# Performance work log

Hardware: AMD Instinct MI355X
Metric: run time of the kernel (lower is better)

## Reference

```python
import jax, jax.numpy as jnp
import numpy as np

N = 50000
E_RAND = 800000
F_IN = 512
HID = 64
HEADS = 4
C = 40
NEG_SLOPE = 0.2  # PyG GATConv default leaky_relu slope


def setup_inputs() -> dict:
    key = jax.random.key(0)
    ks = jax.random.split(key, 12)
    x = jax.random.normal(ks[0], (N, F_IN), dtype=jnp.float32)
    # random edges + self loops (PyG GATConv add_self_loops=True)
    ei_rand = jax.random.randint(ks[1], (2, E_RAND), 0, N, dtype=jnp.int64)
    loops = jnp.broadcast_to(jnp.arange(N, dtype=jnp.int64), (2, N))
    edge_index = jnp.concatenate([ei_rand, loops], axis=1)  # [2, 850000]
    # layer 1: F_IN -> HEADS*HID, concat
    s1 = 1.0 / np.sqrt(F_IN)
    W1 = jax.random.normal(ks[2], (F_IN, HEADS * HID), dtype=jnp.float32) * s1
    a_src1 = jax.random.normal(ks[3], (HEADS, HID), dtype=jnp.float32) * (1.0 / np.sqrt(HID))
    a_dst1 = jax.random.normal(ks[4], (HEADS, HID), dtype=jnp.float32) * (1.0 / np.sqrt(HID))
    b1 = jnp.zeros((HEADS * HID,), dtype=jnp.float32)
    # layer 2: HEADS*HID -> C, 1 head, concat=False
    s2 = 1.0 / np.sqrt(HEADS * HID)
    W2 = jax.random.normal(ks[5], (HEADS * HID, C), dtype=jnp.float32) * s2
    a_src2 = jax.random.normal(ks[6], (1, C), dtype=jnp.float32) * (1.0 / np.sqrt(C))
    a_dst2 = jax.random.normal(ks[7], (1, C), dtype=jnp.float32) * (1.0 / np.sqrt(C))
    b2 = jnp.zeros((C,), dtype=jnp.float32)
    return {"x": x, "edge_index": edge_index, "W1": W1, "a_src1": a_src1,
            "a_dst1": a_dst1, "b1": b1, "W2": W2, "a_src2": a_src2,
            "a_dst2": a_dst2, "b2": b2}


def gat_conv(x, src, dst, W, a_s, a_d, b, concat):
    n = x.shape[0]
    H, D = a_s.shape
    h = (x @ W).reshape(n, H, D)                    # [N,H,D]
    al_s = jnp.einsum('nhd,hd->nh', h, a_s)          # per-node src score
    al_d = jnp.einsum('nhd,hd->nh', h, a_d)          # per-node dst score
    e = jax.nn.leaky_relu(al_s[src] + al_d[dst], NEG_SLOPE)  # [E,H]
    # segment softmax over edges grouped by destination node
    m = jax.ops.segment_max(e, dst, num_segments=n)  # [N,H]
    e = jnp.exp(e - m[dst])
    denom = jax.ops.segment_sum(e, dst, num_segments=n)
    alpha = e / (denom[dst] + 1e-16)                 # [E,H]
    msg = h[src] * alpha[:, :, None]                 # [E,H,D]
    out = jax.ops.segment_sum(msg, dst, num_segments=n)  # [N,H,D]
    out = out.reshape(n, H * D) if concat else out.mean(axis=1)
    return out + b


def reference(x, edge_index, W1, a_src1, a_dst1, b1, W2, a_src2, a_dst2, b2):
    src, dst = edge_index[0], edge_index[1]
    # dropout p=0.6 is identity in eval mode
    h = jax.nn.elu(gat_conv(x, src, dst, W1, a_src1, a_dst1, b1, concat=True))
    out = gat_conv(h, src, dst, W2, a_src2, a_dst2, b2, concat=False)
    return jax.nn.log_softmax(out, axis=1)
```

## Files before the change

kernel.cpp:

```cpp
#include <hip/hip_runtime.h>
#include <math.h>

#define NNODES 50000
#define NPAD 50176
#define FIN 512
#define HID 64
#define HEADS 4
#define HD (HEADS * HID)
#define NCLS 40
#define NCLSP 64
#define NEG_SLOPE 0.2f
#define SBLK 256
#define NSCAN ((NNODES + SBLK - 1) / SBLK)

typedef __attribute__((ext_vector_type(8))) short short8;
typedef __attribute__((ext_vector_type(4))) float f32x4;

static __device__ inline unsigned short f2bf(float f) {
    unsigned int u = __builtin_bit_cast(unsigned int, f);
    unsigned int r = (u + 0x7FFFu + ((u >> 16) & 1u)) >> 16;
    return (unsigned short)r;
}
static __device__ inline float bf2f(unsigned short b) {
    return __builtin_bit_cast(float, (unsigned int)b << 16);
}
static __device__ inline void gload_lds16(const unsigned short* g, unsigned short* l) {
    __builtin_amdgcn_global_load_lds(
        (const __attribute__((address_space(1))) unsigned int*)g,
        (__attribute__((address_space(3))) unsigned int*)l, 16, 0, 0);
}

__global__ __launch_bounds__(256) void xcast_kernel(const float* __restrict__ x,
                                                    unsigned short* __restrict__ xb) {
    const size_t idx = ((size_t)blockIdx.x * 256 + threadIdx.x) * 8;
    if (idx < (size_t)NNODES * FIN) {
        const float4 v0 = *(const float4*)&x[idx];
        const float4 v1 = *(const float4*)&x[idx + 4];
        ushort4 p0, p1;
        p0.x = f2bf(v0.x); p0.y = f2bf(v0.y); p0.z = f2bf(v0.z); p0.w = f2bf(v0.w);
        p1.x = f2bf(v1.x); p1.y = f2bf(v1.y); p1.z = f2bf(v1.z); p1.w = f2bf(v1.w);
        *(ushort4*)&xb[idx] = p0;
        *(ushort4*)&xb[idx + 4] = p1;
    } else {
        const ushort4 z = {0, 0, 0, 0};
        *(ushort4*)&xb[idx] = z;
        *(ushort4*)&xb[idx + 4] = z;
    }
}

__global__ __launch_bounds__(256) void w1t_kernel(const float* __restrict__ W1,
                                                  unsigned short* __restrict__ W1t) {
    const int idx = blockIdx.x * 256 + threadIdx.x;
    const int k = idx >> 8;
    const int n = idx & 255;
    W1t[n * FIN + k] = f2bf(W1[idx]);
}

__global__ __launch_bounds__(256) void w2t_kernel(const float* __restrict__ W2,
                                                  unsigned short* __restrict__ W2t) {
    const int idx = blockIdx.x * 256 + threadIdx.x;
    const int n = idx >> 8;
    const int k = idx & 255;
    W2t[n * HD + k] = (n < NCLS) ? f2bf(W2[k * NCLS + n]) : (unsigned short)0;
}

#define BM 64
#define BN 256
#define BK 32

__global__ __launch_bounds__(256) void gemm1_kernel(const unsigned short* __restrict__ xb,
                                                    const unsigned short* __restrict__ W1t,
                                                    const float* __restrict__ a_src,
                                                    const float* __restrict__ a_dst,
                                                    unsigned short* __restrict__ h1,
                                                    float* __restrict__ al_s,
                                                    float* __restrict__ al_d) {
    __shared__ unsigned short As[BM * BK];
    __shared__ unsigned short Bs[BN * BK];
    const int tid = threadIdx.x;
    const int wave = tid >> 6;
    const int lane = tid & 63;
    const int quad = lane >> 4;
    const int col = lane & 15;
    const int m0 = blockIdx.x * BM;
    const int srow = lane >> 2;
    const int skk = (lane & 3) * 8;

    f32x4 acc[4][4] = {};

    for (int k0 = 0; k0 < FIN; k0 += BK) {
        {
            const int r = wave * 16 + srow;
            gload_lds16(&xb[(size_t)(m0 + r) * FIN + k0 + skk], &As[r * BK + skk]);
        }
        #pragma unroll
        for (int c = 0; c < 4; ++c) {
            const int r = c * 64 + wave * 16 + srow;
            gload_lds16(&W1t[(size_t)r * FIN + k0 + skk], &Bs[r * BK + skk]);
        }
        __syncthreads();

        short8 af[4], bf[4];
        #pragma unroll
        for (int i = 0; i < 4; ++i)
            af[i] = *(const short8*)&As[(i * 16 + col) * BK + quad * 8];
        #pragma unroll
        for (int j = 0; j < 4; ++j)
            bf[j] = *(const short8*)&Bs[(wave * 64 + j * 16 + col) * BK + quad * 8];
        #pragma unroll
        for (int i = 0; i < 4; ++i)
            #pragma unroll
            for (int j = 0; j < 4; ++j)
                acc[i][j] = __builtin_amdgcn_mfma_f32_16x16x32_bf16(af[i], bf[j], acc[i][j], 0, 0, 0);
        __syncthreads();
    }

    float asv[4], adv[4];
    #pragma unroll
    for (int j = 0; j < 4; ++j) {
        asv[j] = a_src[wave * 64 + j * 16 + col];
        adv[j] = a_dst[wave * 64 + j * 16 + col];
    }
    #pragma unroll
    for (int i = 0; i < 4; ++i) {
        #pragma unroll
        for (int reg = 0; reg < 4; ++reg) {
            const int row = i * 16 + quad * 4 + reg;
            const int gm = m0 + row;
            float ds = 0.f, dd = 0.f;
            #pragma unroll
            for (int j = 0; j < 4; ++j) {
                const float v = acc[i][j][reg];
                ds = fmaf(v, asv[j], ds);
                dd = fmaf(v, adv[j], dd);
                if (gm < NNODES) {
                    const int gc = wave * 64 + j * 16 + col;
                    h1[(size_t)gm * HD + gc] = f2bf(v);
                }
            }
            #pragma unroll
            for (int off = 1; off < 16; off <<= 1) {
                ds += __shfl_xor(ds, off);
                dd += __shfl_xor(dd, off);
            }
            if (col == 0 && gm < NNODES) {
                al_s[gm * HEADS + wave] = ds;
                al_d[gm * HEADS + wave] = dd;
            }
        }
    }
}

__global__ void deg_kernel(const int* __restrict__ ei, int E, int* __restrict__ deg) {
    const int e = blockIdx.x * 256 + threadIdx.x;
    if (e < E) atomicAdd(&deg[ei[E + e]], 1);
}

__global__ __launch_bounds__(SBLK) void scan1_kernel(const int* __restrict__ deg,
                                                     int* __restrict__ psum,
                                                     int* __restrict__ bsum) {
    __shared__ int ws[4];
    const int t = threadIdx.x;
    const int idx = blockIdx.x * SBLK + t;
    const int lane = t & 63;
    const int w = t >> 6;
    int sv = (idx < NNODES) ? deg[idx] : 0;
    #pragma unroll
    for (int off = 1; off < 64; off <<= 1) {
        const int n = __shfl_up(sv, off);
        if (lane >= off) sv += n;
    }
    if (lane == 63) ws[w] = sv;
    __syncthreads();
    int add = 0;
    for (int i = 0; i < w; ++i) add += ws[i];
    sv += add;
    if (idx < NNODES) psum[idx] = sv;
    if (t == SBLK - 1) bsum[blockIdx.x] = sv;
}

__global__ __launch_bounds__(SBLK) void scan2_kernel(int* __restrict__ bsum,
                                                     int* __restrict__ offsets) {
    __shared__ int ws[4];
    const int t = threadIdx.x;
    const int lane = t & 63;
    const int w = t >> 6;
    int sv = (t < NSCAN) ? bsum[t] : 0;
    #pragma unroll
    for (int off = 1; off < 64; off <<= 1) {
        const int n = __shfl_up(sv, off);
        if (lane >= off) sv += n;
    }
    if (lane == 63) ws[w] = sv;
    __syncthreads();
    int add = 0;
    for (int i = 0; i < w; ++i) add += ws[i];
    sv += add;
    if (t < NSCAN) bsum[t] = sv;
    if (t == SBLK - 1) offsets[NNODES] = sv;
}

__global__ __launch_bounds__(SBLK) void scan3_kernel(const int* __restrict__ deg,
                                                     const int* __restrict__ psum,
                                                     const int* __restrict__ bsum,
                                                     int* __restrict__ offsets) {
    const int b = blockIdx.x;
    const int idx = b * SBLK + threadIdx.x;
    if (idx < NNODES) {
        const int boff = (b > 0) ? bsum[b - 1] : 0;
        offsets[idx] = psum[idx] - deg[idx] + boff;
    }
}

__global__ void scatter_kernel(const int* __restrict__ ei, int E,
                               const int* __restrict__ offsets,
                               int* __restrict__ cursor,
                               int* __restrict__ csr_src) {
    const int e = blockIdx.x * 256 + threadIdx.x;
    if (e < E) {
        const int dst = ei[E + e];
        const int src = ei[e];
        const int pos = offsets[dst] + atomicAdd(&cursor[dst], 1);
        csr_src[pos] = src;
    }
}

__global__ __launch_bounds__(256) void agg1_kernel(const unsigned short* __restrict__ h1,
                                                   const float* __restrict__ al_s,
                                                   const float* __restrict__ al_d,
                                                   const int* __restrict__ offsets,
                                                   const int* __restrict__ csr_src,
                                                   const float* __restrict__ b1,
                                                   unsigned short* __restrict__ h_act) {
    const int node = (blockIdx.x * 256 + threadIdx.x) >> 6;
    const int lane = threadIdx.x & 63;
    const int q = lane >> 4;
    const int fl = lane & 15;
    const int h = fl >> 2;
    const float ad = al_d[node * HEADS + h];
    const int start = offsets[node];
    const int end = offsets[node + 1];
    const int last = end - 1;

    float s = 0.f;
    float acc[16] = {};

    {
        const int idx = start + q;
        const int src0 = csr_src[min(idx, last)];
        float sc = (idx < end) ? al_s[src0 * HEADS + h] : -__builtin_inff();
        short8 v0 = *(const short8*)&h1[(size_t)src0 * HD + fl * 16];
        short8 v1 = *(const short8*)&h1[(size_t)src0 * HD + fl * 16 + 8];

        for (int i = start; i < end; i += 4) {
            const int j = i + 4 + q;
            const int nsrc = csr_src[min(j, last)];
            const float nsc = (j < end) ? al_s[nsrc * HEADS + h] : -__builtin_inff();
            const short8 nv0 = *(const short8*)&h1[(size_t)nsrc * HD + fl * 16];
            const short8 nv1 = *(const short8*)&h1[(size_t)nsrc * HD + fl * 16 + 8];
            float e_ = sc + ad;
            e_ = e_ > 0.f ? e_ : NEG_SLOPE * e_;
            const float p = __expf(e_);
            s += p;
            #pragma unroll
            for (int k = 0; k < 8; ++k)
                acc[k] = fmaf(p, bf2f((unsigned short)v0[k]), acc[k]);
            #pragma unroll
            for (int k = 0; k < 8; ++k)
                acc[8 + k] = fmaf(p, bf2f((unsigned short)v1[k]), acc[8 + k]);
            sc = nsc; v0 = nv0; v1 = nv1;
        }
    }
    s += __shfl_xor(s, 16);
    s += __shfl_xor(s, 32);
    #pragma unroll
    for (int k = 0; k < 16; ++k) {
        acc[k] += __shfl_xor(acc[k], 16);
        acc[k] += __shfl_xor(acc[k], 32);
    }

    if (q == 0) {
        const float inv = 1.f / (s + 1e-16f);
        float bb[16];
        *(float4*)&bb[0]  = *(const float4*)&b1[fl * 16];
        *(float4*)&bb[4]  = *(const float4*)&b1[fl * 16 + 4];
        *(float4*)&bb[8]  = *(const float4*)&b1[fl * 16 + 8];
        *(float4*)&bb[12] = *(const float4*)&b1[fl * 16 + 12];
        short8 ob0, ob1;
        #pragma unroll
        for (int k = 0; k < 8; ++k) {
            const float o0 = acc[k] * inv + bb[k];
            const float o1 = acc[8 + k] * inv + bb[8 + k];
            const float e0 = o0 > 0.f ? o0 : expm1f(o0);
            const float e1 = o1 > 0.f ? o1 : expm1f(o1);
            ob0[k] = (short)f2bf(e0);
            ob1[k] = (short)f2bf(e1);
        }
        *(short8*)&h_act[(size_t)node * HD + fl * 16] = ob0;
        *(short8*)&h_act[(size_t)node * HD + fl * 16 + 8] = ob1;
    }
}

#define G2M 64
#define BSTRIDE 264

__global__ __launch_bounds__(256) void gemm2_kernel(const unsigned short* __restrict__ h_act,
                                                    const unsigned short* __restrict__ W2t,
                                                    const float* __restrict__ a_s2,
                                                    const float* __restrict__ a_d2,
                                                    unsigned short* __restrict__ h2,
                                                    float* __restrict__ al_s,
                                                    float* __restrict__ al_d) {
    __shared__ unsigned short Bt[NCLSP][BSTRIDE];
    const int tid = threadIdx.x;
    const int wave = tid >> 6;
    const int lane = tid & 63;
    const int quad = lane >> 4;
    const int col = lane & 15;
    const int m0 = blockIdx.x * G2M;

    #pragma unroll
    for (int it = 0; it < 8; ++it) {
        const int ch = it * 256 + tid;
        const int n = ch >> 5;
        const int c8 = (ch & 31) * 8;
        *(uint4*)&Bt[n][c8] = *(const uint4*)&W2t[(size_t)n * HD + c8];
    }

    const int rowm = m0 + wave * 16 + col;
    const int arow = min(rowm, NNODES - 1);
    short8 af[8];
    #pragma unroll
    for (int ks = 0; ks < 8; ++ks)
        af[ks] = *(const short8*)&h_act[(size_t)arow * HD + ks * 32 + quad * 8];

    __syncthreads();

    f32x4 acc[4] = {};
    #pragma unroll
    for (int j = 0; j < 4; ++j) {
        #pragma unroll
        for (int ks = 0; ks < 8; ++ks) {
            const short8 bfr = *(const short8*)&Bt[j * 16 + col][ks * 32 + quad * 8];
            acc[j] = __builtin_amdgcn_mfma_f32_16x16x32_bf16(af[ks], bfr, acc[j], 0, 0, 0);
        }
    }

    float ps[4] = {0.f, 0.f, 0.f, 0.f};
    float pd[4] = {0.f, 0.f, 0.f, 0.f};
    #pragma unroll
    for (int j = 0; j < 4; ++j) {
        const int c = j * 16 + col;
        const bool cv = c < NCLS;
        const float asc = cv ? a_s2[c] : 0.f;
        const float adc = cv ? a_d2[c] : 0.f;
        #pragma unroll
        for (int reg = 0; reg < 4; ++reg) {
            const float v = acc[j][reg];
            ps[reg] += v * asc;
            pd[reg] += v * adc;
            const int node = m0 + wave * 16 + quad * 4 + reg;
            if (node < NNODES)
                h2[(size_t)node * NCLSP + c] = f2bf(v);
        }
    }
    #pragma unroll
    for (int reg = 0; reg < 4; ++reg) {
        #pragma unroll
        for (int off = 1; off < 16; off <<= 1) {
            ps[reg] += __shfl_xor(ps[reg], off);
            pd[reg] += __shfl_xor(pd[reg], off);
        }
    }
    if (col == 0) {
        #pragma unroll
        for (int reg = 0; reg < 4; ++reg) {
            const int node = m0 + wave * 16 + quad * 4 + reg;
            if (node < NNODES) {
                al_s[node] = ps[reg];
                al_d[node] = pd[reg];
            }
        }
    }
}

__global__ __launch_bounds__(256) void agg2_kernel(const unsigned short* __restrict__ h2,
                                                   const float* __restrict__ al_s,
                                                   const float* __restrict__ al_d,
                                                   const int* __restrict__ offsets,
                                                   const int* __restrict__ csr_src,
                                                   const float* __restrict__ b2,
                                                   float* __restrict__ out) {
    const int node = (blockIdx.x * 256 + threadIdx.x) >> 6;
    const int lane = threadIdx.x & 63;
    const int oct = lane >> 3;
    const int fl = lane & 7;
    const float ad = al_d[node];
    const int start = offsets[node];
    const int end = offsets[node + 1];
    const int last = end - 1;

    float s = 0.f;
    float acc[8] = {};

    {
        const int idx = start + oct;
        const int src0 = csr_src[min(idx, last)];
        float sc = (idx < end) ? al_s[src0] : -__builtin_inff();
        short8 v = *(const short8*)&h2[(size_t)src0 * NCLSP + fl * 8];

        for (int i = start; i < end; i += 8) {
            const int j = i + 8 + oct;
            const int nsrc = csr_src[min(j, last)];
            const float nsc = (j < end) ? al_s[nsrc] : -__builtin_inff();
            const short8 nv = *(const short8*)&h2[(size_t)nsrc * NCLSP + fl * 8];
            float e_ = sc + ad;
            e_ = e_ > 0.f ? e_ : NEG_SLOPE * e_;
            const float p = __expf(e_);
            s += p;
            #pragma unroll
            for (int k = 0; k < 8; ++k)
                acc[k] = fmaf(p, bf2f((unsigned short)v[k]), acc[k]);
            sc = nsc; v = nv;
        }
    }
    s += __shfl_xor(s, 8);
    s += __shfl_xor(s, 16);
    s += __shfl_xor(s, 32);
    #pragma unroll
    for (int k = 0; k < 8; ++k) {
        acc[k] += __shfl_xor(acc[k], 8);
        acc[k] += __shfl_xor(acc[k], 16);
        acc[k] += __shfl_xor(acc[k], 32);
    }

    if (oct == 0) {
        const float inv = 1.f / (s + 1e-16f);
        float o[8];
        float mx = -1e30f;
        #pragma unroll
        for (int k = 0; k < 8; ++k) {
            const int c = fl * 8 + k;
            const float bc = (c < NCLS) ? b2[c] : 0.f;
            o[k] = acc[k] * inv + bc;
            if (c < NCLS) mx = fmaxf(mx, o[k]);
        }
        #pragma unroll
        for (int off = 1; off < 8; off <<= 1) mx = fmaxf(mx, __shfl_xor(mx, off));
        float ex = 0.f;
        #pragma unroll
        for (int k = 0; k < 8; ++k) {
            const int c = fl * 8 + k;
            if (c < NCLS) ex += __expf(o[k] - mx);
        }
        #pragma unroll
        for (int off = 1; off < 8; off <<= 1) ex += __shfl_xor(ex, off);
        const float lse = mx + logf(ex);
        if (fl < 5) {
            float4 r0, r1;
            r0.x = o[0] - lse; r0.y = o[1] - lse; r0.z = o[2] - lse; r0.w = o[3] - lse;
            r1.x = o[4] - lse; r1.y = o[5] - lse; r1.z = o[6] - lse; r1.w = o[7] - lse;
            *(float4*)&out[(size_t)node * NCLS + fl * 8] = r0;
            *(float4*)&out[(size_t)node * NCLS + fl * 8 + 4] = r1;
        }
    }
}

extern "C" void kernel_launch(void* const* d_in, const int* in_sizes, int n_in,
                              void* d_out, int out_size, void* d_ws, size_t ws_size,
                              hipStream_t stream) {
    const float* x      = (const float*)d_in[0];
    const int*   ei     = (const int*)d_in[1];
    const float* W1     = (const float*)d_in[2];
    const float* a_src1 = (const float*)d_in[3];
    const float* a_dst1 = (const float*)d_in[4];
    const float* b1     = (const float*)d_in[5];
    const float* W2     = (const float*)d_in[6];
    const float* a_src2 = (const float*)d_in[7];
    const float* a_dst2 = (const float*)d_in[8];
    const float* b2     = (const float*)d_in[9];
    float* out = (float*)d_out;
    const int E = in_sizes[1] / 2;

    char* ws = (char*)d_ws;
    size_t off = 0;
    auto alloc = [&](size_t bytes) -> char* {
        char* p = ws + off;
        off += (bytes + 255) & ~(size_t)255;
        return p;
    };
    unsigned short* xb    = (unsigned short*)alloc((size_t)NPAD * FIN * 2);
    unsigned short* W1t   = (unsigned short*)alloc((size_t)FIN * HD * 2);
    unsigned short* W2t   = (unsigned short*)alloc((size_t)NCLSP * HD * 2);
    unsigned short* h1    = (unsigned short*)alloc((size_t)NNODES * HD * 2);
    unsigned short* h_act = (unsigned short*)alloc((size_t)NNODES * HD * 2);
    unsigned short* h2    = (unsigned short*)alloc((size_t)NNODES * NCLSP * 2);
    float* al_s1  = (float*)alloc((size_t)NNODES * HEADS * 4);
    float* al_d1  = (float*)alloc((size_t)NNODES * HEADS * 4);
    float* al_s2  = (float*)alloc((size_t)NNODES * 4);
    float* al_d2  = (float*)alloc((size_t)NNODES * 4);
    int*   deg    = (int*)alloc((size_t)NNODES * 4);
    int*   psum   = (int*)alloc((size_t)NNODES * 4);
    int*   bsum   = (int*)alloc((size_t)SBLK * 4);
    int*   offs   = (int*)alloc((size_t)(NNODES + 1) * 4);
    int*   cursor = (int*)alloc((size_t)NNODES * 4);
    int*   csrsrc = (int*)alloc((size_t)E * 4);

    hipMemsetAsync(deg, 0, (size_t)NNODES * 4, stream);
    hipMemsetAsync(cursor, 0, (size_t)NNODES * 4, stream);

    const int eb = (E + 255) / 256;
    xcast_kernel<<<(int)((size_t)NPAD * FIN / 8 / 256), 256, 0, stream>>>(x, xb);
    w1t_kernel<<<FIN * HD / 256, 256, 0, stream>>>(W1, W1t);
    w2t_kernel<<<NCLSP, 256, 0, stream>>>(W2, W2t);
    deg_kernel<<<eb, 256, 0, stream>>>(ei, E, deg);
    scan1_kernel<<<NSCAN, SBLK, 0, stream>>>(deg, psum, bsum);
    scan2_kernel<<<1, SBLK, 0, stream>>>(bsum, offs);
    scan3_kernel<<<NSCAN, SBLK, 0, stream>>>(deg, psum, bsum, offs);
    scatter_kernel<<<eb, 256, 0, stream>>>(ei, E, offs, cursor, csrsrc);

    gemm1_kernel<<<NPAD / BM, 256, 0, stream>>>(xb, W1t, a_src1, a_dst1, h1, al_s1, al_d1);
    agg1_kernel<<<NNODES / 4, 256, 0, stream>>>(h1, al_s1, al_d1, offs, csrsrc, b1, h_act);
    gemm2_kernel<<<(NNODES + G2M - 1) / G2M, 256, 0, stream>>>(h_act, W2t, a_src2, a_dst2, h2, al_s2, al_d2);
    agg2_kernel<<<NNODES / 4, 256, 0, stream>>>(h2, al_s2, al_d2, offs, csrsrc, b2, out);
}
```

Baseline: 427.6 us.

## Fuse preprocessing launches, merge scans, double-buffer gemm1, pad CSR to drop clamps

The cast, weight-transpose and degree-count kernels are merged into one launch, and the two scan phases are merged into a single kernel that each block recomputes redundantly. The two memsets are combined into one by placing deg and cursor next to each other. gemm1 gets double-buffered LDS staging so the next K tile loads while the current one is multiplied. The aggregation kernels drop the min() clamp on CSR reads by zero-padding past the end of the edge list. Together these cut launch count and per-iteration latency, at the cost of more LDS and reads that rely on the padding being present.

```diff
diff --git a/kernel.cpp b/kernel.cpp
--- a/kernel.cpp
+++ b/kernel.cpp
@@ -13,6 +13,11 @@
 #define SBLK 256
 #define NSCAN ((NNODES + SBLK - 1) / SBLK)
 
+#define XBBLK (NPAD * FIN / 8 / 256)
+#define W1TBLK (FIN * HD / 256)
+#define W2TBLK NCLSP
+#define DEGBASE (XBBLK + W1TBLK + W2TBLK)
+
 typedef __attribute__((ext_vector_type(8))) short short8;
 typedef __attribute__((ext_vector_type(4))) float f32x4;
 
@@ -30,38 +35,47 @@
         (__attribute__((address_space(3))) unsigned int*)l, 16, 0, 0);
 }
 
-__global__ __launch_bounds__(256) void xcast_kernel(const float* __restrict__ x,
-                                                    unsigned short* __restrict__ xb) {
-    const size_t idx = ((size_t)blockIdx.x * 256 + threadIdx.x) * 8;
-    if (idx < (size_t)NNODES * FIN) {
-        const float4 v0 = *(const float4*)&x[idx];
-        const float4 v1 = *(const float4*)&x[idx + 4];
-        ushort4 p0, p1;
-        p0.x = f2bf(v0.x); p0.y = f2bf(v0.y); p0.z = f2bf(v0.z); p0.w = f2bf(v0.w);
-        p1.x = f2bf(v1.x); p1.y = f2bf(v1.y); p1.z = f2bf(v1.z); p1.w = f2bf(v1.w);
-        *(ushort4*)&xb[idx] = p0;
-        *(ushort4*)&xb[idx + 4] = p1;
+__global__ __launch_bounds__(256) void pre_kernel(const float* __restrict__ x,
+                                                  unsigned short* __restrict__ xb,
+                                                  const float* __restrict__ W1,
+                                                  unsigned short* __restrict__ W1t,
+                                                  const float* __restrict__ W2,
+                                                  unsigned short* __restrict__ W2t,
+                                                  const int* __restrict__ ei, int E,
+                                                  int* __restrict__ deg,
+                                                  int* __restrict__ csr_pad) {
+    const int b = blockIdx.x;
+    const int tid = threadIdx.x;
+    if (b < XBBLK) {
+        const size_t idx = ((size_t)b * 256 + tid) * 8;
+        if (idx < (size_t)NNODES * FIN) {
+            const float4 v0 = *(const float4*)&x[idx];
+            const float4 v1 = *(const float4*)&x[idx + 4];
+            ushort4 p0, p1;
+            p0.x = f2bf(v0.x); p0.y = f2bf(v0.y); p0.z = f2bf(v0.z); p0.w = f2bf(v0.w);
+            p1.x = f2bf(v1.x); p1.y = f2bf(v1.y); p1.z = f2bf(v1.z); p1.w = f2bf(v1.w);
+            *(ushort4*)&xb[idx] = p0;
+            *(ushort4*)&xb[idx + 4] = p1;
+        } else {
+            const ushort4 z = {0, 0, 0, 0};
+            *(ushort4*)&xb[idx] = z;
+            *(ushort4*)&xb[idx + 4] = z;
+        }
+    } else if (b < XBBLK + W1TBLK) {
+        const int idx = (b - XBBLK) * 256 + tid;
+        const int k = idx >> 8;
+        const int n = idx & 255;
+        W1t[n * FIN + k] = f2bf(W1[idx]);
+    } else if (b < DEGBASE) {
+        const int idx = (b - XBBLK - W1TBLK) * 256 + tid;
+        const int n = idx >> 8;
+        const int k = idx & 255;
+        W2t[n * HD + k] = (n < NCLS) ? f2bf(W2[k * NCLS + n]) : (unsigned short)0;
     } else {
-        const ushort4 z = {0, 0, 0, 0};
-        *(ushort4*)&xb[idx] = z;
-        *(ushort4*)&xb[idx + 4] = z;
-    }
-}
-
-__global__ __launch_bounds__(256) void w1t_kernel(const float* __restrict__ W1,
-                                                  unsigned short* __restrict__ W1t) {
-    const int idx = blockIdx.x * 256 + threadIdx.x;
-    const int k = idx >> 8;
-    const int n = idx & 255;
-    W1t[n * FIN + k] = f2bf(W1[idx]);
-}
-
-__global__ __launch_bounds__(256) void w2t_kernel(const float* __restrict__ W2,
-                                                  unsigned short* __restrict__ W2t) {
-    const int idx = blockIdx.x * 256 + threadIdx.x;
-    const int n = idx >> 8;
-    const int k = idx & 255;
-    W2t[n * HD + k] = (n < NCLS) ? f2bf(W2[k * NCLS + n]) : (unsigned short)0;
+        const int e = (b - DEGBASE) * 256 + tid;
+        if (e < E) atomicAdd(&deg[ei[E + e]], 1);
+        if (b == DEGBASE && tid < 64) csr_pad[tid] = 0;
+    }
 }
 
 #define BM 64
@@ -75,8 +89,8 @@
                                                     unsigned short* __restrict__ h1,
                                                     float* __restrict__ al_s,
                                                     float* __restrict__ al_d) {
-    __shared__ unsigned short As[BM * BK];
-    __shared__ unsigned short Bs[BN * BK];
+    __shared__ unsigned short As[2][BM * BK];
+    __shared__ unsigned short Bs[2][BN * BK];
     const int tid = threadIdx.x;
     const int wave = tid >> 6;
     const int lane = tid & 63;
@@ -88,32 +102,40 @@
 
     f32x4 acc[4][4] = {};
 
-    for (int k0 = 0; k0 < FIN; k0 += BK) {
-        {
-            const int r = wave * 16 + srow;
-            gload_lds16(&xb[(size_t)(m0 + r) * FIN + k0 + skk], &As[r * BK + skk]);
-        }
+    auto stage = [&](int buf, int k0) {
+        const int r = wave * 16 + srow;
+        gload_lds16(&xb[(size_t)(m0 + r) * FIN + k0 + skk], &As[buf][r * BK + skk]);
         #pragma unroll
         for (int c = 0; c < 4; ++c) {
-            const int r = c * 64 + wave * 16 + srow;
-            gload_lds16(&W1t[(size_t)r * FIN + k0 + skk], &Bs[r * BK + skk]);
-        }
-        __syncthreads();
-
-        short8 af[4], bf[4];
+            const int rr = c * 64 + wave * 16 + srow;
+            gload_lds16(&W1t[(size_t)rr * FIN + k0 + skk], &Bs[buf][rr * BK + skk]);
+        }
+    };
+    auto compute = [&](int buf) {
+        short8 af[4], bfv[4];
         #pragma unroll
         for (int i = 0; i < 4; ++i)
-            af[i] = *(const short8*)&As[(i * 16 + col) * BK + quad * 8];
+            af[i] = *(const short8*)&As[buf][(i * 16 + col) * BK + quad * 8];
         #pragma unroll
         for (int j = 0; j < 4; ++j)
-            bf[j] = *(const short8*)&Bs[(wave * 64 + j * 16 + col) * BK + quad * 8];
+            bfv[j] = *(const short8*)&Bs[buf][(wave * 64 + j * 16 + col) * BK + quad * 8];
         #pragma unroll
         for (int i = 0; i < 4; ++i)
             #pragma unroll
             for (int j = 0; j < 4; ++j)
-                acc[i][j] = __builtin_amdgcn_mfma_f32_16x16x32_bf16(af[i], bf[j], acc[i][j], 0, 0, 0);
+                acc[i][j] = __builtin_amdgcn_mfma_f32_16x16x32_bf16(af[i], bfv[j], acc[i][j], 0, 0, 0);
+    };
+
+    stage(0, 0);
+    __syncthreads();
+    int cur = 0;
+    for (int k0 = BK; k0 < FIN; k0 += BK) {
+        stage(cur ^ 1, k0);
+        compute(cur);
         __syncthreads();
-    }
+        cur ^= 1;
+    }
+    compute(cur);
 
     float asv[4], adv[4];
     #pragma unroll
@@ -151,11 +173,6 @@
     }
 }
 
-__global__ void deg_kernel(const int* __restrict__ ei, int E, int* __restrict__ deg) {
-    const int e = blockIdx.x * 256 + threadIdx.x;
-    if (e < E) atomicAdd(&deg[ei[E + e]], 1);
-}
-
 __global__ __launch_bounds__(SBLK) void scan1_kernel(const int* __restrict__ deg,
                                                      int* __restrict__ psum,
                                                      int* __restrict__ bsum) {
@@ -179,9 +196,12 @@
     if (t == SBLK - 1) bsum[blockIdx.x] = sv;
 }
 
-__global__ __launch_bounds__(SBLK) void scan2_kernel(int* __restrict__ bsum,
-                                                     int* __restrict__ offsets) {
+__global__ __launch_bounds__(SBLK) void scan23_kernel(const int* __restrict__ deg,
+                                                      const int* __restrict__ psum,
+                                                      const int* __restrict__ bsum,
+                                                      int* __restrict__ offsets) {
     __shared__ int ws[4];
+    __shared__ int sc[NSCAN];
     const int t = threadIdx.x;
     const int lane = t & 63;
     const int w = t >> 6;
@@ -196,20 +216,12 @@
     int add = 0;
     for (int i = 0; i < w; ++i) add += ws[i];
     sv += add;
-    if (t < NSCAN) bsum[t] = sv;
-    if (t == SBLK - 1) offsets[NNODES] = sv;
-}
-
-__global__ __launch_bounds__(SBLK) void scan3_kernel(const int* __restrict__ deg,
-                                                     const int* __restrict__ psum,
-                                                     const int* __restrict__ bsum,
-                                                     int* __restrict__ offsets) {
-    const int b = blockIdx.x;
-    const int idx = b * SBLK + threadIdx.x;
-    if (idx < NNODES) {
-        const int boff = (b > 0) ? bsum[b - 1] : 0;
-        offsets[idx] = psum[idx] - deg[idx] + boff;
-    }
+    if (t < NSCAN) sc[t] = sv;
+    __syncthreads();
+    const int idx = blockIdx.x * SBLK + t;
+    const int boff = (blockIdx.x > 0) ? sc[blockIdx.x - 1] : 0;
+    if (idx < NNODES) offsets[idx] = psum[idx] - deg[idx] + boff;
+    if (blockIdx.x == 0 && t == 0) offsets[NNODES] = sc[NSCAN - 1];
 }
 
 __global__ void scatter_kernel(const int* __restrict__ ei, int E,
@@ -240,21 +252,20 @@
     const float ad = al_d[node * HEADS + h];
     const int start = offsets[node];
     const int end = offsets[node + 1];
-    const int last = end - 1;
 
     float s = 0.f;
     float acc[16] = {};
 
     {
         const int idx = start + q;
-        const int src0 = csr_src[min(idx, last)];
+        const int src0 = csr_src[idx];
         float sc = (idx < end) ? al_s[src0 * HEADS + h] : -__builtin_inff();
         short8 v0 = *(const short8*)&h1[(size_t)src0 * HD + fl * 16];
         short8 v1 = *(const short8*)&h1[(size_t)src0 * HD + fl * 16 + 8];
 
         for (int i = start; i < end; i += 4) {
             const int j = i + 4 + q;
-            const int nsrc = csr_src[min(j, last)];
+            const int nsrc = csr_src[j];
             const float nsc = (j < end) ? al_s[nsrc * HEADS + h] : -__builtin_inff();
             const short8 nv0 = *(const short8*)&h1[(size_t)nsrc * HD + fl * 16];
             const short8 nv1 = *(const short8*)&h1[(size_t)nsrc * HD + fl * 16 + 8];
@@ -398,20 +409,19 @@
     const float ad = al_d[node];
     const int start = offsets[node];
     const int end = offsets[node + 1];
-    const int last = end - 1;
 
     float s = 0.f;
     float acc[8] = {};
 
     {
         const int idx = start + oct;
-        const int src0 = csr_src[min(idx, last)];
+        const int src0 = csr_src[idx];
         float sc = (idx < end) ? al_s[src0] : -__builtin_inff();
         short8 v = *(const short8*)&h2[(size_t)src0 * NCLSP + fl * 8];
 
         for (int i = start; i < end; i += 8) {
             const int j = i + 8 + oct;
-            const int nsrc = csr_src[min(j, last)];
+            const int nsrc = csr_src[j];
             const float nsc = (j < end) ? al_s[nsrc] : -__builtin_inff();
             const short8 nv = *(const short8*)&h2[(size_t)nsrc * NCLSP + fl * 8];
             float e_ = sc + ad;
@@ -500,23 +510,19 @@
     float* al_s2  = (float*)alloc((size_t)NNODES * 4);
     float* al_d2  = (float*)alloc((size_t)NNODES * 4);
     int*   deg    = (int*)alloc((size_t)NNODES * 4);
+    int*   cursor = (int*)alloc((size_t)NNODES * 4);
     int*   psum   = (int*)alloc((size_t)NNODES * 4);
     int*   bsum   = (int*)alloc((size_t)SBLK * 4);
     int*   offs   = (int*)alloc((size_t)(NNODES + 1) * 4);
-    int*   cursor = (int*)alloc((size_t)NNODES * 4);
-    int*   csrsrc = (int*)alloc((size_t)E * 4);
-
-    hipMemsetAsync(deg, 0, (size_t)NNODES * 4, stream);
-    hipMemsetAsync(cursor, 0, (size_t)NNODES * 4, stream);
+    int*   csrsrc = (int*)alloc((size_t)E * 4 + 256);
+
+    const size_t degpad = ((size_t)NNODES * 4 + 255) & ~(size_t)255;
+    hipMemsetAsync(deg, 0, degpad + (size_t)NNODES * 4, stream);
 
     const int eb = (E + 255) / 256;
-    xcast_kernel<<<(int)((size_t)NPAD * FIN / 8 / 256), 256, 0, stream>>>(x, xb);
-    w1t_kernel<<<FIN * HD / 256, 256, 0, stream>>>(W1, W1t);
-    w2t_kernel<<<NCLSP, 256, 0, stream>>>(W2, W2t);
-    deg_kernel<<<eb, 256, 0, stream>>>(ei, E, deg);
+    pre_kernel<<<DEGBASE + eb, 256, 0, stream>>>(x, xb, W1, W1t, W2, W2t, ei, E, deg, csrsrc + E);
     scan1_kernel<<<NSCAN, SBLK, 0, stream>>>(deg, psum, bsum);
-    scan2_kernel<<<1, SBLK, 0, stream>>>(bsum, offs);
-    scan3_kernel<<<NSCAN, SBLK, 0, stream>>>(deg, psum, bsum, offs);
+    scan23_kernel<<<NSCAN, SBLK, 0, stream>>>(deg, psum, bsum, offs);
     scatter_kernel<<<eb, 256, 0, stream>>>(ei, E, offs, cursor, csrsrc);
 
     gemm1_kernel<<<NPAD / BM, 256, 0, stream>>>(xb, W1t, a_src1, a_dst1, h1, al_s1, al_d1);
```

After: 408.4 us. 1.05x faster.
